# Performance work log

Measured on AMD Instinct MI355X. Metric: run time of the kernel, lower is better.

The kernel has to match this reference:

```python
import jax, jax.numpy as jnp
import numpy as np
from jax import lax


def _dw_temporal(x, w):
    # x: (n, c, T, H, W); w: (c, 1, k, 1, 1) depthwise (groups=c) temporal conv
    pad = (w.shape[2] - 1) // 2
    return lax.conv_general_dilated(
        x, w, window_strides=(1, 1, 1),
        padding=[(pad, pad), (0, 0), (0, 0)],
        dimension_numbers=('NCDHW', 'OIDHW', 'NCDHW'),
        feature_group_count=x.shape[1])


def _conv2d_3x3(x, w):
    return lax.conv_general_dilated(
        x, w, window_strides=(1, 1), padding=[(1, 1), (1, 1)],
        dimension_numbers=('NCHW', 'OIHW', 'NCHW'))


def setup_inputs() -> dict:
    key = jax.random.key(0)
    kx, kw = jax.random.split(key)
    C, T, NB, H, W = 256, 8, 8, 56, 56
    c_dy, c_sta = C // 16, 3 * C // 16  # 16, 48
    x = jax.random.normal(kx, (NB * T, C, H, W), jnp.float32)
    # temporal depthwise weights exactly per weight_init()
    w11 = np.ones((c_dy, 1, 1, 1, 1), np.float32)
    w13 = np.zeros((c_dy, 1, 3, 1, 1), np.float32)
    w13[:c_dy // 2, 0, 0] = 1.0; w13[c_dy // 2:, 0, 2] = 1.0
    w15 = np.zeros((c_dy, 1, 5, 1, 1), np.float32)
    w15[:c_dy // 2, 0, :2] = 1.0; w15[c_dy // 2:, 0, 3:] = 1.0
    w17 = np.zeros((c_dy, 1, 7, 1, 1), np.float32)
    w17[:c_dy // 2, 0, :3] = 1.0; w17[c_dy // 2:, 0, 4:] = 1.0
    w21 = np.ones((c_sta, 1, 1, 1, 1), np.float32)
    w23 = np.zeros((c_sta, 1, 3, 1, 1), np.float32); w23[:, 0, 1] = 1.0
    w25 = np.zeros((c_sta, 1, 5, 1, 1), np.float32); w25[:, 0, 2] = 1.0
    w27 = np.zeros((c_sta, 1, 7, 1, 1), np.float32); w27[:, 0, 3] = 1.0
    # net.weight (C, C, 3, 3), then sliced as in weight_init
    weight2d = jax.random.normal(kw, (C, C, 3, 3), jnp.float32) * 0.05
    w2d1 = weight2d[:C // 4, :C // 4]
    w2d2 = weight2d[C // 4:, C // 4:]
    return dict(
        x=x,
        w11=jnp.asarray(w11), w13=jnp.asarray(w13), w15=jnp.asarray(w15), w17=jnp.asarray(w17),
        w21=jnp.asarray(w21), w23=jnp.asarray(w23), w25=jnp.asarray(w25), w27=jnp.asarray(w27),
        w2d1=w2d1, w2d2=w2d2, n_segment=8)


def reference(x, w11, w13, w15, w17, w21, w23, w25, w27, w2d1, w2d2, n_segment):
    nt, c, h, w = x.shape
    n = nt // n_segment
    c_dy, c_sta = w11.shape[0], w21.shape[0]
    # (nt,c,h,w) -> (n, c, T, h, w)
    xt = x.reshape(n, n_segment, c, h, w).transpose(0, 2, 1, 3, 4)
    sizes = [c_dy] * 4 + [c_sta] * 4
    ws = [w11, w13, w15, w17, w21, w23, w25, w27]
    parts, start = [], 0
    for wk, sz in zip(ws, sizes):
        parts.append(_dw_temporal(xt[:, start:start + sz], wk))
        start += sz
    y = jnp.concatenate(parts, axis=1)            # (n, c, T, h, w)
    y = y.transpose(0, 2, 1, 3, 4).reshape(nt, c, h, w)
    c1 = c // 4
    y1 = _conv2d_3x3(y[:, :c1], w2d1)
    y2 = _conv2d_3x3(y[:, c1:], w2d2)
    return jnp.concatenate([y1, y2], axis=1)      # (nt, c, h, w), stride=1
```

## Files before the change

kernel.cpp:

```cpp
#include <hip/hip_runtime.h>
#include <hip/hip_bf16.h>
#include <stdint.h>

using bf16x8 = __attribute__((ext_vector_type(8))) short;
using f32x4  = __attribute__((ext_vector_type(4))) float;

#define HP 58
#define WP 58

typedef __attribute__((address_space(1))) const unsigned int guint;
typedef __attribute__((address_space(3))) unsigned int       luint;
__device__ __forceinline__ void gload16(const unsigned short* g, unsigned short* l) {
  __builtin_amdgcn_global_load_lds((guint*)g, (luint*)l, 16, 0, 0);
}

__global__ __launch_bounds__(256) void zero_ring(uint4* __restrict__ ypad) {
  uint4 z; z.x = z.y = z.z = z.w = 0u;
  int i = blockIdx.x * blockDim.x + threadIdx.x;
  int v = i & 31;
  int pr = i >> 5;
  int b = pr / 228;
  int r = pr - b * 228;
  int h, w;
  if (r < 58)       { h = 0;  w = r; }
  else if (r < 116) { h = 57; w = r - 58; }
  else { int rr = r - 116; h = 1 + (rr >> 1); w = (rr & 1) * 57; }
  ypad[(((long)b * HP + h) * WP + w) * 32 + v] = z;
}

__global__ void wtab_prep(const float* __restrict__ w11, const float* __restrict__ w13,
                          const float* __restrict__ w15, const float* __restrict__ w17,
                          const float* __restrict__ w21, const float* __restrict__ w23,
                          const float* __restrict__ w25, const float* __restrict__ w27,
                          float* __restrict__ wtab) {
  int c = threadIdx.x;
  float tv[8];
  #pragma unroll
  for (int j = 0; j < 8; ++j) tv[j] = 0.f;
  const float* wg; int K, cloc;
  if (c < 64) {
    int g = c >> 4; cloc = c & 15; K = 2 * g + 1;
    wg = (g == 0) ? w11 : (g == 1) ? w13 : (g == 2) ? w15 : w17;
  } else {
    int g = (c - 64) / 48; cloc = (c - 64) - g * 48; K = 2 * g + 1;
    wg = (g == 0) ? w21 : (g == 1) ? w23 : (g == 2) ? w25 : w27;
  }
  int P = (K - 1) >> 1;
  for (int k = 0; k < K; ++k) tv[3 + k - P] = wg[cloc * K + k];
  #pragma unroll
  for (int j = 0; j < 8; ++j) wtab[c * 8 + j] = tv[j];
}

__global__ __launch_bounds__(256) void wprep(const float* __restrict__ w,
                                             unsigned short* __restrict__ out, int Cg) {
  int n = 9 * Cg * Cg;
  int stride = gridDim.x * blockDim.x;
  for (int i = blockIdx.x * blockDim.x + threadIdx.x; i < n; i += stride) {
    int kpos = i / (Cg * Cg);
    int r = i - kpos * Cg * Cg;
    int co = r / Cg;
    int ci = r - co * Cg;
    __hip_bfloat16 v = __float2bfloat16(w[(co * Cg + ci) * 9 + kpos]);
    out[(kpos * Cg + co) * Cg + ci] = *reinterpret_cast<unsigned short*>(&v);
  }
}

__global__ __launch_bounds__(256) void temporal_stage(
    const float* __restrict__ x, const float* __restrict__ wtab,
    unsigned short* __restrict__ ypad)
{
  __shared__ float Ls[128][57];
  int bid = blockIdx.x;
  int b = bid / 56;
  int h = bid - b * 56;
  int t = b & 7;
  int tid = threadIdx.x;

  for (int half = 0; half < 2; ++half) {
    int cbase = half * 128;
    for (int idx = tid; idx < 128 * 56; idx += 256) {
      int cl = idx / 56;
      int w_ = idx - cl * 56;
      int c = cbase + cl;
      const float* wt = wtab + c * 8;
      const float* xp = x + ((long)b * 256 + c) * 3136 + h * 56 + w_;
      float acc = 0.f;
      #pragma unroll
      for (int j = 0; j < 7; ++j) {
        int tt = t + j - 3;
        int dtc = (tt < 0 ? 0 : (tt > 7 ? 7 : tt)) - t;
        float wj = wt[j];
        if (tt < 0 || tt > 7) wj = 0.f;
        acc += wj * xp[(long)dtc * 802816];
      }
      Ls[cl][w_] = acc;
    }
    __syncthreads();
    for (int idx = tid; idx < 56 * 128; idx += 256) {
      int w_ = idx >> 7;
      int cl = idx & 127;
      __hip_bfloat16 v = __float2bfloat16(Ls[cl][w_]);
      ypad[(((long)b * HP + (h + 1)) * WP + (w_ + 1)) * 256 + cbase + cl] =
          *reinterpret_cast<unsigned short*>(&v);
    }
    __syncthreads();
  }
}

template<int NKC>
__global__ __launch_bounds__(256, 2) void conv_gemm3(
    const unsigned short* __restrict__ ypad,
    const unsigned short* __restrict__ wb,
    float* __restrict__ out,
    int co_base, int ci_base)
{
  constexpr int Cg  = NKC * 64;
  constexpr int NCH = 9 * NKC;
  constexpr int NWG = 784 * NKC;

  __shared__ __align__(16) unsigned short As0[256][64];
  __shared__ __align__(16) unsigned short Bs0[64][64];
  __shared__ __align__(16) unsigned short As1[256][64];
  __shared__ __align__(16) unsigned short Bs1[64][64];

  int tid = threadIdx.x;

  int gid = blockIdx.x;
  int wg  = (gid & 7) * (NWG >> 3) + (gid >> 3);
  int ny   = wg % NKC;
  int tile = wg / NKC;
  int p0   = tile * 256;

  int l    = tid & 63;
  int w    = tid >> 6;
  int sub  = l >> 3;
  int slot = l & 7;

  const unsigned short* aptr[8];
  #pragma unroll
  for (int q = 0; q < 8; ++q) {
    int r  = w * 64 + q * 8 + sub;
    int gp = p0 + r;
    int b  = gp / 3136;
    int p  = gp - b * 3136;
    int ph = p / 56;
    int pw = p - ph * 56;
    aptr[q] = ypad + (((long)b * HP + ph) * WP + pw) * 256 + ci_base + slot * 8;
  }
  const unsigned short* bptr[2];
  #pragma unroll
  for (int q = 0; q < 2; ++q) {
    int r = w * 16 + q * 8 + sub;
    bptr[q] = wb + (long)(ny * 64 + r) * Cg + slot * 8;
  }

  auto stage = [&](int ch, unsigned short (*A)[64], unsigned short (*B)[64]) {
    int kpos = ch / NKC;
    int kc   = ch - kpos * NKC;
    int kh   = kpos / 3;
    int kw   = kpos - kh * 3;
    long aoff = ((long)kh * WP + kw) * 256 + kc * 64;
    #pragma unroll
    for (int q = 0; q < 8; ++q)
      gload16(aptr[q] + aoff, &A[w * 64 + q * 8][0]);
    long boff = (long)kpos * Cg * Cg + kc * 64;
    #pragma unroll
    for (int q = 0; q < 2; ++q)
      gload16(bptr[q] + boff, &B[w * 16 + q * 8][0]);
  };

  int l15  = l & 15;
  int quad = l >> 4;
  int qk   = quad * 8;
  int mi   = w * 64;

  f32x4 acc[4][4];
  #pragma unroll
  for (int i = 0; i < 4; ++i)
    #pragma unroll
    for (int j = 0; j < 4; ++j) acc[i][j] = (f32x4){0.f, 0.f, 0.f, 0.f};

  auto compute = [&](const unsigned short (*A)[64], const unsigned short (*B)[64]) {
    #pragma unroll
    for (int kk = 0; kk < 2; ++kk) {
      int ko = kk * 32 + qk;
      bf16x8 a0 = *reinterpret_cast<const bf16x8*>(&A[mi      + l15][ko]);
      bf16x8 a1 = *reinterpret_cast<const bf16x8*>(&A[mi + 16 + l15][ko]);
      bf16x8 a2 = *reinterpret_cast<const bf16x8*>(&A[mi + 32 + l15][ko]);
      bf16x8 a3 = *reinterpret_cast<const bf16x8*>(&A[mi + 48 + l15][ko]);
      bf16x8 b0 = *reinterpret_cast<const bf16x8*>(&B[     l15][ko]);
      bf16x8 b1 = *reinterpret_cast<const bf16x8*>(&B[16 + l15][ko]);
      bf16x8 b2 = *reinterpret_cast<const bf16x8*>(&B[32 + l15][ko]);
      bf16x8 b3 = *reinterpret_cast<const bf16x8*>(&B[48 + l15][ko]);
      acc[0][0] = __builtin_amdgcn_mfma_f32_16x16x32_bf16(a0, b0, acc[0][0], 0, 0, 0);
      acc[0][1] = __builtin_amdgcn_mfma_f32_16x16x32_bf16(a0, b1, acc[0][1], 0, 0, 0);
      acc[0][2] = __builtin_amdgcn_mfma_f32_16x16x32_bf16(a0, b2, acc[0][2], 0, 0, 0);
      acc[0][3] = __builtin_amdgcn_mfma_f32_16x16x32_bf16(a0, b3, acc[0][3], 0, 0, 0);
      acc[1][0] = __builtin_amdgcn_mfma_f32_16x16x32_bf16(a1, b0, acc[1][0], 0, 0, 0);
      acc[1][1] = __builtin_amdgcn_mfma_f32_16x16x32_bf16(a1, b1, acc[1][1], 0, 0, 0);
      acc[1][2] = __builtin_amdgcn_mfma_f32_16x16x32_bf16(a1, b2, acc[1][2], 0, 0, 0);
      acc[1][3] = __builtin_amdgcn_mfma_f32_16x16x32_bf16(a1, b3, acc[1][3], 0, 0, 0);
      acc[2][0] = __builtin_amdgcn_mfma_f32_16x16x32_bf16(a2, b0, acc[2][0], 0, 0, 0);
      acc[2][1] = __builtin_amdgcn_mfma_f32_16x16x32_bf16(a2, b1, acc[2][1], 0, 0, 0);
      acc[2][2] = __builtin_amdgcn_mfma_f32_16x16x32_bf16(a2, b2, acc[2][2], 0, 0, 0);
      acc[2][3] = __builtin_amdgcn_mfma_f32_16x16x32_bf16(a2, b3, acc[2][3], 0, 0, 0);
      acc[3][0] = __builtin_amdgcn_mfma_f32_16x16x32_bf16(a3, b0, acc[3][0], 0, 0, 0);
      acc[3][1] = __builtin_amdgcn_mfma_f32_16x16x32_bf16(a3, b1, acc[3][1], 0, 0, 0);
      acc[3][2] = __builtin_amdgcn_mfma_f32_16x16x32_bf16(a3, b2, acc[3][2], 0, 0, 0);
      acc[3][3] = __builtin_amdgcn_mfma_f32_16x16x32_bf16(a3, b3, acc[3][3], 0, 0, 0);
    }
  };

  stage(0, As0, Bs0);
  __syncthreads();
  for (int ch = 0; ch < NCH; ch += 2) {
    if (ch + 1 < NCH) stage(ch + 1, As1, Bs1);
    compute(As0, Bs0);
    __syncthreads();
    if (ch + 1 < NCH) {
      if (ch + 2 < NCH) stage(ch + 2, As0, Bs0);
      compute(As1, Bs1);
      __syncthreads();
    }
  }

  #pragma unroll
  for (int i = 0; i < 4; ++i) {
    int gp0 = p0 + mi + i * 16 + quad * 4;
    int b   = gp0 / 3136;
    int p   = gp0 - b * 3136;
    #pragma unroll
    for (int j = 0; j < 4; ++j) {
      int co = co_base + ny * 64 + j * 16 + l15;
      float* ob = out + ((long)b * 256 + co) * 3136 + p;
      #pragma unroll
      for (int r = 0; r < 4; ++r) ob[r] = acc[i][j][r];
    }
  }
}

extern "C" void kernel_launch(void* const* d_in, const int* in_sizes, int n_in,
                              void* d_out, int out_size, void* d_ws, size_t ws_size,
                              hipStream_t stream) {
  const float* x    = (const float*)d_in[0];
  const float* w11  = (const float*)d_in[1];
  const float* w13  = (const float*)d_in[2];
  const float* w15  = (const float*)d_in[3];
  const float* w17  = (const float*)d_in[4];
  const float* w21  = (const float*)d_in[5];
  const float* w23  = (const float*)d_in[6];
  const float* w25  = (const float*)d_in[7];
  const float* w27  = (const float*)d_in[8];
  const float* w2d1 = (const float*)d_in[9];
  const float* w2d2 = (const float*)d_in[10];
  float* out = (float*)d_out;

  unsigned short* ypad = (unsigned short*)d_ws;
  size_t ypad_elems = (size_t)64 * HP * WP * 256;
  unsigned short* wb1 = ypad + ypad_elems;
  unsigned short* wb2 = wb1 + 9 * 64 * 64;

  float* wtab = out;

  hipLaunchKernelGGL(wtab_prep, dim3(1), dim3(256), 0, stream,
                     w11, w13, w15, w17, w21, w23, w25, w27, wtab);
  hipLaunchKernelGGL(zero_ring, dim3(1824), dim3(256), 0, stream, (uint4*)ypad);
  hipLaunchKernelGGL(wprep, dim3(32),  dim3(256), 0, stream, w2d1, wb1, 64);
  hipLaunchKernelGGL(wprep, dim3(256), dim3(256), 0, stream, w2d2, wb2, 192);
  hipLaunchKernelGGL(temporal_stage, dim3(64 * 56), dim3(256), 0, stream, x, wtab, ypad);
  hipLaunchKernelGGL((conv_gemm3<1>), dim3(784),      dim3(256), 0, stream, ypad, wb1, out, 0, 0);
  hipLaunchKernelGGL((conv_gemm3<3>), dim3(784 * 3),  dim3(256), 0, stream, ypad, wb2, out, 64, 64);
}
```

Before: 708.8 us.

## Tile temporal stage over all frames in LDS and XOR-swizzle GEMM LDS tiles

The temporal stage now loads all 8 frames of a 32-channel, one-row slab into shared memory once with float4 reads, then computes the 7-tap temporal filter from LDS. This avoids re-reading each input element up to 7 times from global memory. Separately, the conv GEMM applies an XOR swizzle to the 16-byte column slot of A and B tiles, both on global_load_lds and on the MFMA operand reads, to cut LDS bank conflicts. The ypad writes are now 2-byte scattered stores per channel with only 32 contiguous channels, which may coalesce worse than before.

```diff
diff --git a/kernel.cpp b/kernel.cpp
--- a/kernel.cpp
+++ b/kernel.cpp
@@ -65,50 +65,58 @@
   }
 }
 
-__global__ __launch_bounds__(256) void temporal_stage(
+__global__ __launch_bounds__(256, 2) void temporal_stage2(
     const float* __restrict__ x, const float* __restrict__ wtab,
     unsigned short* __restrict__ ypad)
 {
-  __shared__ float Ls[128][57];
+  __shared__ float Ls[8][32][58];
+
   int bid = blockIdx.x;
-  int b = bid / 56;
-  int h = bid - b * 56;
-  int t = b & 7;
+  int h   = bid % 56;
+  int nce = bid / 56;
+  int n   = nce >> 3;
+  int ce  = nce & 7;
   int tid = threadIdx.x;
 
-  for (int half = 0; half < 2; ++half) {
-    int cbase = half * 128;
-    for (int idx = tid; idx < 128 * 56; idx += 256) {
-      int cl = idx / 56;
-      int w_ = idx - cl * 56;
-      int c = cbase + cl;
-      const float* wt = wtab + c * 8;
-      const float* xp = x + ((long)b * 256 + c) * 3136 + h * 56 + w_;
-      float acc = 0.f;
-      #pragma unroll
-      for (int j = 0; j < 7; ++j) {
-        int tt = t + j - 3;
-        int dtc = (tt < 0 ? 0 : (tt > 7 ? 7 : tt)) - t;
-        float wj = wt[j];
-        if (tt < 0 || tt > 7) wj = 0.f;
-        acc += wj * xp[(long)dtc * 802816];
-      }
-      Ls[cl][w_] = acc;
-    }
-    __syncthreads();
-    for (int idx = tid; idx < 56 * 128; idx += 256) {
-      int w_ = idx >> 7;
-      int cl = idx & 127;
-      __hip_bfloat16 v = __float2bfloat16(Ls[cl][w_]);
-      ypad[(((long)b * HP + (h + 1)) * WP + (w_ + 1)) * 256 + cbase + cl] =
-          *reinterpret_cast<unsigned short*>(&v);
-    }
-    __syncthreads();
+  for (int i = tid; i < 3584; i += 256) {
+    int t = i / 448;
+    int r = i - t * 448;
+    int c = r / 14;
+    int f = r - c * 14;
+    const float4* src = reinterpret_cast<const float4*>(
+        x + (((long)(n * 8 + t) * 256) + ce * 32 + c) * 3136 + h * 56 + f * 4);
+    float4 v = *src;
+    *reinterpret_cast<float2*>(&Ls[t][c][f * 4])     = make_float2(v.x, v.y);
+    *reinterpret_cast<float2*>(&Ls[t][c][f * 4 + 2]) = make_float2(v.z, v.w);
+  }
+  __syncthreads();
+
+  int c  = tid & 31;
+  int pi = tid >> 5;
+  int cg = ce * 32 + c;
+  float wt[7];
+  #pragma unroll
+  for (int j = 0; j < 7; ++j) wt[j] = wtab[cg * 8 + j];
+
+  for (int k = pi; k < 448; k += 8) {
+    int t = k / 56;
+    int w = k - t * 56;
+    float acc = 0.f;
+    #pragma unroll
+    for (int j = 0; j < 7; ++j) {
+      int tt  = t + j - 3;
+      int ttc = tt < 0 ? 0 : (tt > 7 ? 7 : tt);
+      float wj = (tt < 0 || tt > 7) ? 0.f : wt[j];
+      acc += wj * Ls[ttc][c][w];
+    }
+    __hip_bfloat16 v = __float2bfloat16(acc);
+    ypad[(((long)(n * 8 + t) * HP + (h + 1)) * WP + (w + 1)) * 256 + cg] =
+        *reinterpret_cast<unsigned short*>(&v);
   }
 }
 
 template<int NKC>
-__global__ __launch_bounds__(256, 2) void conv_gemm3(
+__global__ __launch_bounds__(256, 2) void conv_gemm4(
     const unsigned short* __restrict__ ypad,
     const unsigned short* __restrict__ wb,
     float* __restrict__ out,
@@ -131,10 +139,10 @@
   int tile = wg / NKC;
   int p0   = tile * 256;
 
-  int l    = tid & 63;
-  int w    = tid >> 6;
-  int sub  = l >> 3;
-  int slot = l & 7;
+  int l   = tid & 63;
+  int w   = tid >> 6;
+  int sub = l >> 3;
+  int swz = (l & 7) ^ sub;
 
   const unsigned short* aptr[8];
   #pragma unroll
@@ -145,13 +153,13 @@
     int p  = gp - b * 3136;
     int ph = p / 56;
     int pw = p - ph * 56;
-    aptr[q] = ypad + (((long)b * HP + ph) * WP + pw) * 256 + ci_base + slot * 8;
+    aptr[q] = ypad + (((long)b * HP + ph) * WP + pw) * 256 + ci_base + swz * 8;
   }
   const unsigned short* bptr[2];
   #pragma unroll
   for (int q = 0; q < 2; ++q) {
     int r = w * 16 + q * 8 + sub;
-    bptr[q] = wb + (long)(ny * 64 + r) * Cg + slot * 8;
+    bptr[q] = wb + (long)(ny * 64 + r) * Cg + swz * 8;
   }
 
   auto stage = [&](int ch, unsigned short (*A)[64], unsigned short (*B)[64]) {
@@ -171,7 +179,7 @@
 
   int l15  = l & 15;
   int quad = l >> 4;
-  int qk   = quad * 8;
+  int axor = l15 & 7;
   int mi   = w * 64;
 
   f32x4 acc[4][4];
@@ -183,15 +191,15 @@
   auto compute = [&](const unsigned short (*A)[64], const unsigned short (*B)[64]) {
     #pragma unroll
     for (int kk = 0; kk < 2; ++kk) {
-      int ko = kk * 32 + qk;
-      bf16x8 a0 = *reinterpret_cast<const bf16x8*>(&A[mi      + l15][ko]);
-      bf16x8 a1 = *reinterpret_cast<const bf16x8*>(&A[mi + 16 + l15][ko]);
-      bf16x8 a2 = *reinterpret_cast<const bf16x8*>(&A[mi + 32 + l15][ko]);
-      bf16x8 a3 = *reinterpret_cast<const bf16x8*>(&A[mi + 48 + l15][ko]);
-      bf16x8 b0 = *reinterpret_cast<const bf16x8*>(&B[     l15][ko]);
-      bf16x8 b1 = *reinterpret_cast<const bf16x8*>(&B[16 + l15][ko]);
-      bf16x8 b2 = *reinterpret_cast<const bf16x8*>(&B[32 + l15][ko]);
-      bf16x8 b3 = *reinterpret_cast<const bf16x8*>(&B[48 + l15][ko]);
+      int soff = ((kk * 4 + quad) ^ axor) * 8;
+      bf16x8 a0 = *reinterpret_cast<const bf16x8*>(&A[mi      + l15][soff]);
+      bf16x8 a1 = *reinterpret_cast<const bf16x8*>(&A[mi + 16 + l15][soff]);
+      bf16x8 a2 = *reinterpret_cast<const bf16x8*>(&A[mi + 32 + l15][soff]);
+      bf16x8 a3 = *reinterpret_cast<const bf16x8*>(&A[mi + 48 + l15][soff]);
+      bf16x8 b0 = *reinterpret_cast<const bf16x8*>(&B[     l15][soff]);
+      bf16x8 b1 = *reinterpret_cast<const bf16x8*>(&B[16 + l15][soff]);
+      bf16x8 b2 = *reinterpret_cast<const bf16x8*>(&B[32 + l15][soff]);
+      bf16x8 b3 = *reinterpret_cast<const bf16x8*>(&B[48 + l15][soff]);
       acc[0][0] = __builtin_amdgcn_mfma_f32_16x16x32_bf16(a0, b0, acc[0][0], 0, 0, 0);
       acc[0][1] = __builtin_amdgcn_mfma_f32_16x16x32_bf16(a0, b1, acc[0][1], 0, 0, 0);
       acc[0][2] = __builtin_amdgcn_mfma_f32_16x16x32_bf16(a0, b2, acc[0][2], 0, 0, 0);
@@ -267,7 +275,7 @@
   hipLaunchKernelGGL(zero_ring, dim3(1824), dim3(256), 0, stream, (uint4*)ypad);
   hipLaunchKernelGGL(wprep, dim3(32),  dim3(256), 0, stream, w2d1, wb1, 64);
   hipLaunchKernelGGL(wprep, dim3(256), dim3(256), 0, stream, w2d2, wb2, 192);
-  hipLaunchKernelGGL(temporal_stage, dim3(64 * 56), dim3(256), 0, stream, x, wtab, ypad);
-  hipLaunchKernelGGL((conv_gemm3<1>), dim3(784),      dim3(256), 0, stream, ypad, wb1, out, 0, 0);
-  hipLaunchKernelGGL((conv_gemm3<3>), dim3(784 * 3),  dim3(256), 0, stream, ypad, wb2, out, 64, 64);
-}
+  hipLaunchKernelGGL(temporal_stage2, dim3(3584), dim3(256), 0, stream, x, wtab, ypad);
+  hipLaunchKernelGGL((conv_gemm4<1>), dim3(784),     dim3(256), 0, stream, ypad, wb1, out, 0, 0);
+  hipLaunchKernelGGL((conv_gemm4<3>), dim3(784 * 3), dim3(256), 0, stream, ypad, wb2, out, 64, 64);
+}
```

New measurement: 631.8 us. -10.9%, faster.
